# Performance work log

Hardware: AMD Instinct MI355X
Metric: run time of the kernel (lower is better)

Reference implementation:

```python
import jax, jax.numpy as jnp
import numpy as np
import math

B, T, D = 4, 2048, 1024
NHEAD = 16
HEAD_DIM = D // NHEAD
MAX_REL = 16  # max_relative_position default


def setup_inputs() -> dict:
    key = jax.random.key(0)
    ks = jax.random.split(key, 10)
    s = 1.0 / math.sqrt(D)
    inp = {
        "x": jax.random.normal(ks[0], (B, T, D), dtype=jnp.float32),
        "Wq": jax.random.normal(ks[1], (D, D), dtype=jnp.float32) * s,
        "bq": jnp.zeros((D,), dtype=jnp.float32),
        "Wk": jax.random.normal(ks[2], (D, D), dtype=jnp.float32) * s,
        "bk": jnp.zeros((D,), dtype=jnp.float32),
        "Wv": jax.random.normal(ks[3], (D, D), dtype=jnp.float32) * s,
        "bv": jnp.zeros((D,), dtype=jnp.float32),
        "rel_bias": jax.random.normal(ks[4], (2 * MAX_REL - 1, NHEAD), dtype=jnp.float32) * 0.02,
        "Wo": jax.random.normal(ks[5], (D, D), dtype=jnp.float32) * s,
        "bo": jnp.zeros((D,), dtype=jnp.float32),
    }
    return inp


def _relative_bias(rel_bias, seq_len):
    # distance matrix clamped to [-(MAX_REL-1), MAX_REL-1], shifted to index table
    r = jnp.arange(seq_len)
    dist = jnp.clip(r[None, :] - r[:, None], -MAX_REL + 1, MAX_REL - 1) + MAX_REL - 1
    # gather: [T, T, H] -> [H, T, T]
    return jnp.transpose(rel_bias[dist], (2, 0, 1))


def reference(x, Wq, bq, Wk, bk, Wv, bv, rel_bias, Wo, bo):
    Bdim, Tdim, Ddim = x.shape
    # torch Linear: x @ W.T + b
    Q = x @ Wq.T + bq
    K = x @ Wk.T + bk
    V = x @ Wv.T + bv
    # [B, H, T, hd]
    Q = Q.reshape(Bdim, Tdim, NHEAD, HEAD_DIM).transpose(0, 2, 1, 3)
    K = K.reshape(Bdim, Tdim, NHEAD, HEAD_DIM).transpose(0, 2, 1, 3)
    V = V.reshape(Bdim, Tdim, NHEAD, HEAD_DIM).transpose(0, 2, 1, 3)
    scores = jnp.einsum("bhqd,bhkd->bhqk", Q, K) / math.sqrt(HEAD_DIM)
    scores = scores + _relative_bias(rel_bias, Tdim)[None]  # [1,H,T,T]
    attn = jax.nn.softmax(scores, axis=-1)
    out = jnp.einsum("bhqk,bhkd->bhqd", attn, V)
    out = out.transpose(0, 2, 1, 3).reshape(Bdim, Tdim, Ddim)
    return out @ Wo.T + bo
```

## Files before the change

### kernel.cpp

```cpp
#include <hip/hip_runtime.h>
#include <stdint.h>
#include <math.h>

typedef unsigned short u16;
typedef __bf16 bf16x8 __attribute__((ext_vector_type(8)));
typedef float f32x4 __attribute__((ext_vector_type(4)));
typedef unsigned short u16x8 __attribute__((ext_vector_type(8)));
typedef unsigned short u16x4 __attribute__((ext_vector_type(4)));

#define BATCH 4
#define SEQT 2048
#define DMODEL 1024
#define NHEAD 16
#define HDIM 64
#define LOG2E 1.44269504f

#define LDS_GLD16(gp, lp)                                                     \
  __builtin_amdgcn_global_load_lds(                                           \
      (const __attribute__((address_space(1))) void*)(gp),                    \
      (__attribute__((address_space(3))) void*)(lp), 16, 0, 0)

static __device__ __forceinline__ u16 f2bf(float f) {
  union { float f; uint32_t u; } c; c.f = f;
  uint32_t u = c.u;
  return (u16)((u + 0x7fffu + ((u >> 16) & 1u)) >> 16);
}

__global__ __launch_bounds__(256) void k_convert(const float* __restrict__ s,
                                                 u16* __restrict__ d, int n4) {
  int i = blockIdx.x * 256 + threadIdx.x;
  if (i >= n4) return;
  float4 v = ((const float4*)s)[i];
  u16x4 o = {f2bf(v.x), f2bf(v.y), f2bf(v.z), f2bf(v.w)};
  ((u16x4*)d)[i] = o;
}

__global__ __launch_bounds__(256) void k_gemm_qkv(
    const u16* __restrict__ A, const u16* __restrict__ W0,
    const u16* __restrict__ W1, const u16* __restrict__ W2,
    const float* __restrict__ b0, const float* __restrict__ b1,
    const float* __restrict__ b2, u16* __restrict__ dq, u16* __restrict__ dk,
    u16* __restrict__ dv) {
  __shared__ u16 As[128 * 64];
  __shared__ u16 Bs[128 * 64];

  const int z = blockIdx.z;
  const u16* Bm = z == 0 ? W0 : (z == 1 ? W1 : W2);
  const float* bias = z == 0 ? b0 : (z == 1 ? b1 : b2);
  u16* dst = z == 0 ? dq : (z == 1 ? dk : dv);

  const int tid = threadIdx.x;
  const int wave = tid >> 6, lane = tid & 63;
  const int quad = lane >> 4, l16 = lane & 15;
  const int wm = wave & 1, wn = wave >> 1;
  const int m0 = blockIdx.x * 128, n0 = blockIdx.y * 128;
  const int lrow = lane >> 3, lcol = (lane & 7) * 8;

  f32x4 acc[4][4] = {};

  for (int kt = 0; kt < 1024; kt += 64) {
    __syncthreads();
    for (int c = 0; c < 4; ++c) {
      int rr = (wave * 4 + c) * 8 + lrow;
      LDS_GLD16(A + (size_t)(m0 + rr) * 1024 + kt + lcol,
                &As[(wave * 4 + c) * 512]);
      LDS_GLD16(Bm + (size_t)(n0 + rr) * 1024 + kt + lcol,
                &Bs[(wave * 4 + c) * 512]);
    }
    __syncthreads();
    for (int kh = 0; kh < 2; ++kh) {
      bf16x8 af[4], bfr[4];
      for (int mt = 0; mt < 4; ++mt)
        af[mt] = *(const bf16x8*)&As[(wm * 64 + mt * 16 + l16) * 64 + kh * 32 +
                                     quad * 8];
      for (int nt = 0; nt < 4; ++nt)
        bfr[nt] = *(const bf16x8*)&Bs[(wn * 64 + nt * 16 + l16) * 64 + kh * 32 +
                                      quad * 8];
      for (int mt = 0; mt < 4; ++mt)
        for (int nt = 0; nt < 4; ++nt)
          acc[mt][nt] = __builtin_amdgcn_mfma_f32_16x16x32_bf16(
              af[mt], bfr[nt], acc[mt][nt], 0, 0, 0);
    }
  }

  for (int mt = 0; mt < 4; ++mt)
    for (int nt = 0; nt < 4; ++nt) {
      int n = n0 + wn * 64 + nt * 16 + l16;
      float bv = bias[n];
      int h = n >> 6, hd = n & 63;
      for (int r = 0; r < 4; ++r) {
        int m = m0 + wm * 64 + mt * 16 + quad * 4 + r;
        int b = m >> 11, t = m & 2047;
        float v = acc[mt][nt][r] + bv;
        dst[(((size_t)b * NHEAD + h) * SEQT + t) * HDIM + hd] = f2bf(v);
      }
    }
}

__global__ __launch_bounds__(256) void k_gemm_proj(const u16* __restrict__ A,
                                                   const u16* __restrict__ Bm,
                                                   const float* __restrict__ bias,
                                                   float* __restrict__ out) {
  __shared__ u16 As[128 * 64];
  __shared__ u16 Bs[128 * 64];

  const int tid = threadIdx.x;
  const int wave = tid >> 6, lane = tid & 63;
  const int quad = lane >> 4, l16 = lane & 15;
  const int wm = wave & 1, wn = wave >> 1;
  const int m0 = blockIdx.x * 128, n0 = blockIdx.y * 128;
  const int lrow = lane >> 3, lcol = (lane & 7) * 8;

  f32x4 acc[4][4] = {};

  for (int kt = 0; kt < 1024; kt += 64) {
    __syncthreads();
    for (int c = 0; c < 4; ++c) {
      int rr = (wave * 4 + c) * 8 + lrow;
      LDS_GLD16(A + (size_t)(m0 + rr) * 1024 + kt + lcol,
                &As[(wave * 4 + c) * 512]);
      LDS_GLD16(Bm + (size_t)(n0 + rr) * 1024 + kt + lcol,
                &Bs[(wave * 4 + c) * 512]);
    }
    __syncthreads();
    for (int kh = 0; kh < 2; ++kh) {
      bf16x8 af[4], bfr[4];
      for (int mt = 0; mt < 4; ++mt)
        af[mt] = *(const bf16x8*)&As[(wm * 64 + mt * 16 + l16) * 64 + kh * 32 +
                                     quad * 8];
      for (int nt = 0; nt < 4; ++nt)
        bfr[nt] = *(const bf16x8*)&Bs[(wn * 64 + nt * 16 + l16) * 64 + kh * 32 +
                                      quad * 8];
      for (int mt = 0; mt < 4; ++mt)
        for (int nt = 0; nt < 4; ++nt)
          acc[mt][nt] = __builtin_amdgcn_mfma_f32_16x16x32_bf16(
              af[mt], bfr[nt], acc[mt][nt], 0, 0, 0);
    }
  }

  for (int mt = 0; mt < 4; ++mt)
    for (int nt = 0; nt < 4; ++nt) {
      int n = n0 + wn * 64 + nt * 16 + l16;
      float bv = bias[n];
      for (int r = 0; r < 4; ++r) {
        int m = m0 + wm * 64 + mt * 16 + quad * 4 + r;
        out[(size_t)m * 1024 + n] = acc[mt][nt][r] + bv;
      }
    }
}

__global__ __launch_bounds__(256) void k_attn(const u16* __restrict__ Qb,
                                              const u16* __restrict__ Kb,
                                              const u16* __restrict__ Vb,
                                              const float* __restrict__ relb,
                                              u16* __restrict__ Obf) {
  __shared__ u16 Ks[64 * 64];
  __shared__ u16 VTs[64 * 72];
  __shared__ u16 Ps[4][32 * 72];
  __shared__ float biasL[32];

  const int tid = threadIdx.x;
  const int wave = tid >> 6, lane = tid & 63;
  const int quad = lane >> 4, l16 = lane & 15;
  const int qt = blockIdx.x;
  const int bh = blockIdx.y;
  const int h = bh & (NHEAD - 1);
  const size_t base = (size_t)bh * SEQT * HDIM;
  const int q0 = qt * 128;

  if (tid < 31) biasL[tid] = relb[tid * NHEAD + h] * LOG2E;
  const float bLo = relb[0 * NHEAD + h] * LOG2E;
  const float bHi = relb[30 * NHEAD + h] * LOG2E;
  const float CL = 0.125f * LOG2E;

  bf16x8 aq[2][2];
  for (int rg = 0; rg < 2; ++rg) {
    const u16* qp = Qb + base + (size_t)(q0 + wave * 32 + rg * 16 + l16) * HDIM;
    aq[rg][0] = *(const bf16x8*)(qp + quad * 8);
    aq[rg][1] = *(const bf16x8*)(qp + 32 + quad * 8);
  }

  f32x4 Oacc[2][4] = {};
  float lsum[2][4] = {};

  const int kp = tid >> 3;
  const int dg = tid & 7;
  uint32_t* VT32 = (uint32_t*)VTs;

  for (int kt2 = 0; kt2 < 32; ++kt2) {
    const int k0 = kt2 * 64;
    __syncthreads();

    for (int c = 0; c < 2; ++c) {
      int rl = lane >> 3;
      int row = (wave * 2 + c) * 8 + rl;
      int gb = (lane & 7) ^ rl;
      LDS_GLD16(Kb + base + (size_t)(k0 + row) * HDIM + gb * 8,
                &Ks[(wave * 2 + c) * 512]);
    }

    {
      const u16* vp = Vb + base + (size_t)(k0 + 2 * kp) * HDIM + dg * 8;
      u16x8 v0 = *(const u16x8*)vp;
      u16x8 v1 = *(const u16x8*)(vp + HDIM);
      const uint32_t* a32 = (const uint32_t*)&v0;
      const uint32_t* b32 = (const uint32_t*)&v1;
      int col = (((kp >> 2) ^ dg) << 2) + (kp & 3);
      for (int j2 = 0; j2 < 4; ++j2) {
        uint32_t lo = __builtin_amdgcn_perm(a32[j2], b32[j2], 0x01000504u);
        uint32_t hi = __builtin_amdgcn_perm(a32[j2], b32[j2], 0x03020706u);
        int d0 = dg * 8 + 2 * j2;
        VT32[d0 * 36 + col] = lo;
        VT32[(d0 + 1) * 36 + col] = hi;
      }
    }
    __syncthreads();

    const int dt = k0 - q0;
    const bool generalTile = (dt > -78) && (dt < 142);
    const float ubias = (dt < 0) ? bLo : bHi;

    for (int nt = 0; nt < 4; ++nt) {
      int krow = nt * 16 + l16;
      bf16x8 bk0 = *(const bf16x8*)&Ks[krow * 64 + ((quad ^ (l16 & 7)) << 3)];
      bf16x8 bk1 =
          *(const bf16x8*)&Ks[krow * 64 + (((quad + 4) ^ (l16 & 7)) << 3)];
      for (int rg = 0; rg < 2; ++rg) {
        f32x4 s = {};
        s = __builtin_amdgcn_mfma_f32_16x16x32_bf16(aq[rg][0], bk0, s, 0, 0, 0);
        s = __builtin_amdgcn_mfma_f32_16x16x32_bf16(aq[rg][1], bk1, s, 0, 0, 0);
        const int rbase = rg * 16 + quad * 4;
        if (generalTile) {
          int dbase = (k0 + nt * 16 + l16) - (q0 + wave * 32 + rbase);
          for (int r = 0; r < 4; ++r) {
            int d = dbase - r;
            d = d < -15 ? -15 : (d > 15 ? 15 : d);
            float p = __builtin_amdgcn_exp2f(fmaf(s[r], CL, biasL[d + 15]));
            lsum[rg][r] += p;
            int rl = rbase + r;
            int sblk = (2 * nt + (l16 >> 3)) ^ (rl >> 2);
            Ps[wave][rl * 72 + sblk * 8 + (l16 & 7)] = f2bf(p);
          }
        } else {
          for (int r = 0; r < 4; ++r) {
            float p = __builtin_amdgcn_exp2f(fmaf(s[r], CL, ubias));
            lsum[rg][r] += p;
            int rl = rbase + r;
            int sblk = (2 * nt + (l16 >> 3)) ^ (rl >> 2);
            Ps[wave][rl * 72 + sblk * 8 + (l16 & 7)] = f2bf(p);
          }
        }
      }
    }

    bf16x8 ap[2][2];
    for (int rg = 0; rg < 2; ++rg) {
      int rl = rg * 16 + l16;
      int sb0 = (quad ^ (rl >> 2)) << 3;
      int sb1 = ((quad + 4) ^ (rl >> 2)) << 3;
      ap[rg][0] = *(const bf16x8*)&Ps[wave][rl * 72 + sb0];
      ap[rg][1] = *(const bf16x8*)&Ps[wave][rl * 72 + sb1];
    }
    for (int nt = 0; nt < 4; ++nt) {
      int d = nt * 16 + l16;
      int g = 2 * nt + (l16 >> 3);
      bf16x8 bv0 = *(const bf16x8*)&VTs[d * 72 + ((quad ^ g) << 3)];
      bf16x8 bv1 = *(const bf16x8*)&VTs[d * 72 + (((quad + 4) ^ g) << 3)];
      for (int rg = 0; rg < 2; ++rg) {
        Oacc[rg][nt] = __builtin_amdgcn_mfma_f32_16x16x32_bf16(
            ap[rg][0], bv0, Oacc[rg][nt], 0, 0, 0);
        Oacc[rg][nt] = __builtin_amdgcn_mfma_f32_16x16x32_bf16(
            ap[rg][1], bv1, Oacc[rg][nt], 0, 0, 0);
      }
    }
  }

  for (int rg = 0; rg < 2; ++rg)
    for (int r = 0; r < 4; ++r) {
      float v = lsum[rg][r];
      v += __shfl_xor(v, 1, 64);
      v += __shfl_xor(v, 2, 64);
      v += __shfl_xor(v, 4, 64);
      v += __shfl_xor(v, 8, 64);
      lsum[rg][r] = 1.0f / v;
    }

  const int b = bh >> 4;
  for (int rg = 0; rg < 2; ++rg)
    for (int nt = 0; nt < 4; ++nt)
      for (int r = 0; r < 4; ++r) {
        int t = q0 + wave * 32 + rg * 16 + quad * 4 + r;
        float o = Oacc[rg][nt][r] * lsum[rg][r];
        Obf[((size_t)(b * SEQT + t)) * DMODEL + h * HDIM + nt * 16 + l16] =
            f2bf(o);
      }
}

extern "C" void kernel_launch(void* const* d_in, const int* in_sizes, int n_in,
                              void* d_out, int out_size, void* d_ws,
                              size_t ws_size, hipStream_t stream) {
  const float* x = (const float*)d_in[0];
  const float* Wq = (const float*)d_in[1];
  const float* bq = (const float*)d_in[2];
  const float* Wk = (const float*)d_in[3];
  const float* bk = (const float*)d_in[4];
  const float* Wv = (const float*)d_in[5];
  const float* bv = (const float*)d_in[6];
  const float* relb = (const float*)d_in[7];
  const float* Wo = (const float*)d_in[8];
  const float* bo = (const float*)d_in[9];
  float* out = (float*)d_out;

  char* ws = (char*)d_ws;
  const size_t SZ_X = (size_t)BATCH * SEQT * DMODEL * 2;
  const size_t SZ_W = (size_t)DMODEL * DMODEL * 2;
  u16* xbf = (u16*)(ws);
  u16* Wqb = (u16*)(ws + SZ_X);
  u16* Wkb = (u16*)(ws + SZ_X + SZ_W);
  u16* Wvb = (u16*)(ws + SZ_X + 2 * SZ_W);
  u16* Wob = (u16*)(ws + SZ_X + 3 * SZ_W);
  u16* Qb = (u16*)(ws + SZ_X + 4 * SZ_W);
  u16* Kb = (u16*)(ws + 2 * SZ_X + 4 * SZ_W);
  u16* Vb = (u16*)(ws + 3 * SZ_X + 4 * SZ_W);
  u16* Obf = (u16*)(ws + 4 * SZ_X + 4 * SZ_W);

  const int NX = BATCH * SEQT * DMODEL;
  const int NW = DMODEL * DMODEL;
  k_convert<<<NX / 4 / 256, 256, 0, stream>>>(x, xbf, NX / 4);
  k_convert<<<NW / 4 / 256, 256, 0, stream>>>(Wq, Wqb, NW / 4);
  k_convert<<<NW / 4 / 256, 256, 0, stream>>>(Wk, Wkb, NW / 4);
  k_convert<<<NW / 4 / 256, 256, 0, stream>>>(Wv, Wvb, NW / 4);
  k_convert<<<NW / 4 / 256, 256, 0, stream>>>(Wo, Wob, NW / 4);

  k_gemm_qkv<<<dim3(64, 8, 3), 256, 0, stream>>>(xbf, Wqb, Wkb, Wvb, bq, bk,
                                                 bv, Qb, Kb, Vb);
  k_attn<<<dim3(16, 64), 256, 0, stream>>>(Qb, Kb, Vb, relb, Obf);
  k_gemm_proj<<<dim3(64, 8), 256, 0, stream>>>(Obf, Wob, bo, out);
}
```

Baseline: 352.2 us.

## Transpose attention MFMA operands so each lane holds contiguous keys and packed stores

Swaps the A/B operands of the QK^T and PV MFMAs so the accumulators hold S^T and O^T. Each lane then owns four consecutive keys (or head dims) for one query. This lets P be written to LDS as packed 8-byte bf16 pairs, makes the row sum a cheap two-step cross-quad shuffle, and vectorizes the output store. It also replaces round-to-nearest-even bf16 conversion with a cheaper round-half-up in the QKV epilogue and the P/O packing, which slightly changes rounding. The per-tile bias/clamp branch is moved to per-16x16 subtile granularity, and the removed P swizzle may add LDS bank conflicts.

```diff
diff --git a/kernel.cpp b/kernel.cpp
--- a/kernel.cpp
+++ b/kernel.cpp
@@ -5,6 +5,7 @@
 typedef unsigned short u16;
 typedef __bf16 bf16x8 __attribute__((ext_vector_type(8)));
 typedef float f32x4 __attribute__((ext_vector_type(4)));
+typedef float f32x2 __attribute__((ext_vector_type(2)));
 typedef unsigned short u16x8 __attribute__((ext_vector_type(8)));
 typedef unsigned short u16x4 __attribute__((ext_vector_type(4)));
 
@@ -24,6 +25,14 @@
   union { float f; uint32_t u; } c; c.f = f;
   uint32_t u = c.u;
   return (u16)((u + 0x7fffu + ((u >> 16) & 1u)) >> 16);
+}
+static __device__ __forceinline__ u16 f2bf_fast(float f) {
+  union { float f; uint32_t u; } c; c.f = f;
+  return (u16)((c.u + 0x8000u) >> 16);
+}
+static __device__ __forceinline__ uint32_t pkbf(float a, float b) {
+  union { float f; uint32_t u; } ca, cb; ca.f = a; cb.f = b;
+  return __builtin_amdgcn_perm(cb.u + 0x8000u, ca.u + 0x8000u, 0x07060302u);
 }
 
 __global__ __launch_bounds__(256) void k_convert(const float* __restrict__ s,
@@ -92,7 +101,7 @@
         int m = m0 + wm * 64 + mt * 16 + quad * 4 + r;
         int b = m >> 11, t = m & 2047;
         float v = acc[mt][nt][r] + bv;
-        dst[(((size_t)b * NHEAD + h) * SEQT + t) * HDIM + hd] = f2bf(v);
+        dst[(((size_t)b * NHEAD + h) * SEQT + t) * HDIM + hd] = f2bf_fast(v);
       }
     }
 }
@@ -167,24 +176,25 @@
   const int h = bh & (NHEAD - 1);
   const size_t base = (size_t)bh * SEQT * HDIM;
   const int q0 = qt * 128;
+  const int qbase = q0 + wave * 32;
 
   if (tid < 31) biasL[tid] = relb[tid * NHEAD + h] * LOG2E;
   const float bLo = relb[0 * NHEAD + h] * LOG2E;
   const float bHi = relb[30 * NHEAD + h] * LOG2E;
   const float CL = 0.125f * LOG2E;
 
-  bf16x8 aq[2][2];
-  for (int rg = 0; rg < 2; ++rg) {
-    const u16* qp = Qb + base + (size_t)(q0 + wave * 32 + rg * 16 + l16) * HDIM;
-    aq[rg][0] = *(const bf16x8*)(qp + quad * 8);
-    aq[rg][1] = *(const bf16x8*)(qp + 32 + quad * 8);
-  }
-
-  f32x4 Oacc[2][4] = {};
-  float lsum[2][4] = {};
+  bf16x8 bq[2][2];
+  for (int qg = 0; qg < 2; ++qg) {
+    const u16* qp = Qb + base + (size_t)(qbase + qg * 16 + l16) * HDIM;
+    bq[qg][0] = *(const bf16x8*)(qp + quad * 8);
+    bq[qg][1] = *(const bf16x8*)(qp + 32 + quad * 8);
+  }
+
+  f32x4 Oacc[4][2] = {};
+  f32x2 ls2[2] = {};
 
   const int kp = tid >> 3;
-  const int dg = tid & 7;
+  const int dgw = tid & 7;
   uint32_t* VT32 = (uint32_t*)VTs;
 
   for (int kt2 = 0; kt2 < 32; ++kt2) {
@@ -198,102 +208,103 @@
       LDS_GLD16(Kb + base + (size_t)(k0 + row) * HDIM + gb * 8,
                 &Ks[(wave * 2 + c) * 512]);
     }
-
     {
-      const u16* vp = Vb + base + (size_t)(k0 + 2 * kp) * HDIM + dg * 8;
+      const u16* vp = Vb + base + (size_t)(k0 + 2 * kp) * HDIM + dgw * 8;
       u16x8 v0 = *(const u16x8*)vp;
       u16x8 v1 = *(const u16x8*)(vp + HDIM);
       const uint32_t* a32 = (const uint32_t*)&v0;
       const uint32_t* b32 = (const uint32_t*)&v1;
-      int col = (((kp >> 2) ^ dg) << 2) + (kp & 3);
+      int col = (((kp >> 2) ^ dgw) << 2) + (kp & 3);
       for (int j2 = 0; j2 < 4; ++j2) {
         uint32_t lo = __builtin_amdgcn_perm(a32[j2], b32[j2], 0x01000504u);
         uint32_t hi = __builtin_amdgcn_perm(a32[j2], b32[j2], 0x03020706u);
-        int d0 = dg * 8 + 2 * j2;
+        int d0 = dgw * 8 + 2 * j2;
         VT32[d0 * 36 + col] = lo;
         VT32[(d0 + 1) * 36 + col] = hi;
       }
     }
     __syncthreads();
 
-    const int dt = k0 - q0;
-    const bool generalTile = (dt > -78) && (dt < 142);
-    const float ubias = (dt < 0) ? bLo : bHi;
-
-    for (int nt = 0; nt < 4; ++nt) {
-      int krow = nt * 16 + l16;
-      bf16x8 bk0 = *(const bf16x8*)&Ks[krow * 64 + ((quad ^ (l16 & 7)) << 3)];
-      bf16x8 bk1 =
-          *(const bf16x8*)&Ks[krow * 64 + (((quad + 4) ^ (l16 & 7)) << 3)];
-      for (int rg = 0; rg < 2; ++rg) {
+    for (int kg = 0; kg < 4; ++kg) {
+      const int krow = kg * 16 + l16;
+      const int sl = krow & 7;
+      bf16x8 ak0 = *(const bf16x8*)&Ks[krow * 64 + ((quad ^ sl) << 3)];
+      bf16x8 ak1 = *(const bf16x8*)&Ks[krow * 64 + (((quad + 4) ^ sl) << 3)];
+      const int kb = k0 + kg * 16;
+      for (int qg = 0; qg < 2; ++qg) {
         f32x4 s = {};
-        s = __builtin_amdgcn_mfma_f32_16x16x32_bf16(aq[rg][0], bk0, s, 0, 0, 0);
-        s = __builtin_amdgcn_mfma_f32_16x16x32_bf16(aq[rg][1], bk1, s, 0, 0, 0);
-        const int rbase = rg * 16 + quad * 4;
-        if (generalTile) {
-          int dbase = (k0 + nt * 16 + l16) - (q0 + wave * 32 + rbase);
+        s = __builtin_amdgcn_mfma_f32_16x16x32_bf16(ak0, bq[qg][0], s, 0, 0, 0);
+        s = __builtin_amdgcn_mfma_f32_16x16x32_bf16(ak1, bq[qg][1], s, 0, 0, 0);
+        const int qa = qbase + qg * 16;
+        float p0, p1, p2, p3;
+        const int dmin = kb - (qa + 15);
+        const int dmax = kb + 15 - qa;
+        if (dmin >= 15 || dmax <= -15) {
+          const float ub = (dmin >= 15) ? bHi : bLo;
+          p0 = __builtin_amdgcn_exp2f(fmaf(s[0], CL, ub));
+          p1 = __builtin_amdgcn_exp2f(fmaf(s[1], CL, ub));
+          p2 = __builtin_amdgcn_exp2f(fmaf(s[2], CL, ub));
+          p3 = __builtin_amdgcn_exp2f(fmaf(s[3], CL, ub));
+        } else {
+          const int db = kb + quad * 4 - (qa + l16);
+          float pv[4];
           for (int r = 0; r < 4; ++r) {
-            int d = dbase - r;
+            int d = db + r;
             d = d < -15 ? -15 : (d > 15 ? 15 : d);
-            float p = __builtin_amdgcn_exp2f(fmaf(s[r], CL, biasL[d + 15]));
-            lsum[rg][r] += p;
-            int rl = rbase + r;
-            int sblk = (2 * nt + (l16 >> 3)) ^ (rl >> 2);
-            Ps[wave][rl * 72 + sblk * 8 + (l16 & 7)] = f2bf(p);
+            pv[r] = __builtin_amdgcn_exp2f(fmaf(s[r], CL, biasL[d + 15]));
           }
-        } else {
-          for (int r = 0; r < 4; ++r) {
-            float p = __builtin_amdgcn_exp2f(fmaf(s[r], CL, ubias));
-            lsum[rg][r] += p;
-            int rl = rbase + r;
-            int sblk = (2 * nt + (l16 >> 3)) ^ (rl >> 2);
-            Ps[wave][rl * 72 + sblk * 8 + (l16 & 7)] = f2bf(p);
-          }
+          p0 = pv[0]; p1 = pv[1]; p2 = pv[2]; p3 = pv[3];
         }
-      }
-    }
-
-    bf16x8 ap[2][2];
-    for (int rg = 0; rg < 2; ++rg) {
-      int rl = rg * 16 + l16;
-      int sb0 = (quad ^ (rl >> 2)) << 3;
-      int sb1 = ((quad + 4) ^ (rl >> 2)) << 3;
-      ap[rg][0] = *(const bf16x8*)&Ps[wave][rl * 72 + sb0];
-      ap[rg][1] = *(const bf16x8*)&Ps[wave][rl * 72 + sb1];
-    }
-    for (int nt = 0; nt < 4; ++nt) {
-      int d = nt * 16 + l16;
-      int g = 2 * nt + (l16 >> 3);
-      bf16x8 bv0 = *(const bf16x8*)&VTs[d * 72 + ((quad ^ g) << 3)];
-      bf16x8 bv1 = *(const bf16x8*)&VTs[d * 72 + (((quad + 4) ^ g) << 3)];
-      for (int rg = 0; rg < 2; ++rg) {
-        Oacc[rg][nt] = __builtin_amdgcn_mfma_f32_16x16x32_bf16(
-            ap[rg][0], bv0, Oacc[rg][nt], 0, 0, 0);
-        Oacc[rg][nt] = __builtin_amdgcn_mfma_f32_16x16x32_bf16(
-            ap[rg][1], bv1, Oacc[rg][nt], 0, 0, 0);
-      }
-    }
-  }
-
-  for (int rg = 0; rg < 2; ++rg)
-    for (int r = 0; r < 4; ++r) {
-      float v = lsum[rg][r];
-      v += __shfl_xor(v, 1, 64);
-      v += __shfl_xor(v, 2, 64);
-      v += __shfl_xor(v, 4, 64);
-      v += __shfl_xor(v, 8, 64);
-      lsum[rg][r] = 1.0f / v;
-    }
+        f32x2 t01 = {p0, p1}, t23 = {p2, p3};
+        ls2[qg] += t01 + t23;
+        uint2 w;
+        w.x = pkbf(p0, p1);
+        w.y = pkbf(p2, p3);
+        *(uint2*)&Ps[wave][(qg * 16 + l16) * 72 + kg * 16 + quad * 4] = w;
+      }
+    }
+
+    bf16x8 bp[2][2];
+    for (int qg = 0; qg < 2; ++qg)
+      for (int kh = 0; kh < 2; ++kh)
+        bp[qg][kh] = *(const bf16x8*)&Ps[wave][(qg * 16 + l16) * 72 + kh * 32 +
+                                              quad * 8];
+    for (int dg = 0; dg < 4; ++dg) {
+      const int d = dg * 16 + l16;
+      const int g = d >> 3;
+      bf16x8 av0 = *(const bf16x8*)&VTs[d * 72 + ((quad ^ g) << 3)];
+      bf16x8 av1 = *(const bf16x8*)&VTs[d * 72 + (((quad + 4) ^ g) << 3)];
+      for (int qg = 0; qg < 2; ++qg) {
+        Oacc[dg][qg] = __builtin_amdgcn_mfma_f32_16x16x32_bf16(
+            av0, bp[qg][0], Oacc[dg][qg], 0, 0, 0);
+        Oacc[dg][qg] = __builtin_amdgcn_mfma_f32_16x16x32_bf16(
+            av1, bp[qg][1], Oacc[dg][qg], 0, 0, 0);
+      }
+    }
+  }
+
+  float rinv[2];
+  for (int qg = 0; qg < 2; ++qg) {
+    float v = ls2[qg].x + ls2[qg].y;
+    v += __shfl_xor(v, 16, 64);
+    v += __shfl_xor(v, 32, 64);
+    rinv[qg] = 1.0f / v;
+  }
 
   const int b = bh >> 4;
-  for (int rg = 0; rg < 2; ++rg)
-    for (int nt = 0; nt < 4; ++nt)
-      for (int r = 0; r < 4; ++r) {
-        int t = q0 + wave * 32 + rg * 16 + quad * 4 + r;
-        float o = Oacc[rg][nt][r] * lsum[rg][r];
-        Obf[((size_t)(b * SEQT + t)) * DMODEL + h * HDIM + nt * 16 + l16] =
-            f2bf(o);
-      }
+  for (int dg = 0; dg < 4; ++dg)
+    for (int qg = 0; qg < 2; ++qg) {
+      int t = qbase + qg * 16 + l16;
+      float o0 = Oacc[dg][qg][0] * rinv[qg];
+      float o1 = Oacc[dg][qg][1] * rinv[qg];
+      float o2 = Oacc[dg][qg][2] * rinv[qg];
+      float o3 = Oacc[dg][qg][3] * rinv[qg];
+      uint2 w;
+      w.x = pkbf(o0, o1);
+      w.y = pkbf(o2, o3);
+      *(uint2*)(Obf + ((size_t)(b * SEQT + t)) * DMODEL + h * HDIM + dg * 16 +
+                quad * 4) = w;
+    }
 }
 
 extern "C" void kernel_launch(void* const* d_in, const int* in_sizes, int n_in,
```

Result: faster. 343.1 us (-2.6%).
